# Kernel tuning notes

Hardware: AMD Instinct MI355X
Metric: run time of the kernel (lower is better)

## Reference

```python
import jax, jax.numpy as jnp
import numpy as np

N_NODES = 100000
N_EDGES = 3200000
F_IN = 128
HID = 16
N_CLASSES = 32
N_RELS = 20
BN_EPS = 1e-5


def setup_inputs() -> dict:
    key = jax.random.key(0)
    ks = jax.random.split(key, 14)
    inp = {
        'x': jax.random.normal(ks[0], (N_NODES, F_IN), dtype=jnp.float32),
        'edge_index': jax.random.randint(ks[1], (2, N_EDGES), 0, N_NODES, dtype=jnp.int32),
        'edge_type': jax.random.randint(ks[2], (N_EDGES,), 0, N_RELS, dtype=jnp.int32),
        # conv1 params (relation weights, root weight, bias)
        'W1': jax.random.normal(ks[3], (N_RELS, F_IN, HID), dtype=jnp.float32) / np.sqrt(F_IN),
        'root1': jax.random.normal(ks[4], (F_IN, HID), dtype=jnp.float32) / np.sqrt(F_IN),
        'b1': jnp.zeros((HID,), dtype=jnp.float32),
        # bn1
        'gamma1': jnp.ones((HID,), dtype=jnp.float32),
        'beta1': jnp.zeros((HID,), dtype=jnp.float32),
        # conv2 params
        'W2': jax.random.normal(ks[5], (N_RELS, HID, N_CLASSES), dtype=jnp.float32) / np.sqrt(HID),
        'root2': jax.random.normal(ks[6], (HID, N_CLASSES), dtype=jnp.float32) / np.sqrt(HID),
        'b2': jnp.zeros((N_CLASSES,), dtype=jnp.float32),
        # bn2
        'gamma2': jnp.ones((N_CLASSES,), dtype=jnp.float32),
        'beta2': jnp.zeros((N_CLASSES,), dtype=jnp.float32),
    }
    return inp


def rgcn_conv(x, src, dst, etype, W, Wroot, b):
    # h[r] = x @ W_r  -> [R, N, O]; small O keeps this cheap
    h = jnp.einsum('nf,rfo->rno', x, W)
    msg = h[etype, src]  # [E, O] gather of transformed source features
    # per-(relation, dst-node) in-degree for mean aggregation
    cnt = jnp.zeros((W.shape[0], x.shape[0]), x.dtype).at[etype, dst].add(1.0)
    norm = jnp.where(cnt > 0, 1.0 / jnp.maximum(cnt, 1.0), 0.0)
    msg = msg * norm[etype, dst][:, None]
    out = jnp.zeros((x.shape[0], W.shape[-1]), x.dtype).at[dst].add(msg)
    return out + x @ Wroot + b


def batch_norm(x, gamma, beta):
    # training-mode BatchNorm1d: batch statistics, biased variance
    m = x.mean(axis=0)
    v = x.var(axis=0)
    return (x - m) * jax.lax.rsqrt(v + BN_EPS) * gamma + beta


def reference(x, edge_index, edge_type, W1, root1, b1, gamma1, beta1,
              W2, root2, b2, gamma2, beta2):
    src, dst = edge_index[0], edge_index[1]
    h = rgcn_conv(x, src, dst, edge_type, W1, root1, b1)
    h = jax.nn.relu(batch_norm(h, gamma1, beta1))
    # dropout(0.1) treated as identity (eval mode)
    h = rgcn_conv(h, src, dst, edge_type, W2, root2, b2)
    h = jax.nn.relu(batch_norm(h, gamma2, beta2))
    return jax.nn.log_softmax(h, axis=1)
```

## Files before the change

kernel.cpp:

```cpp
#include <hip/hip_runtime.h>
#include <hip/hip_bf16.h>

#define N_NODES 100000
#define N_EDGES 3200000
#define F_IN 128
#define HID 16
#define N_CLASSES 32
#define N_RELS 20
#define BN_EPS 1e-5f
#define N_CELLS (N_NODES * N_RELS)
#define BIN_SHIFT 13
#define BIN_CELLS 8192
#define NBINS ((N_CELLS + BIN_CELLS - 1) / BIN_CELLS)
#define CHUNK 8192
#define NBLK ((N_EDGES + CHUNK - 1) / CHUNK)
#define HM_N (NBINS * NBLK)
#define HM_NB ((HM_N + 2047) / 2048)
#define SLOT_ELEMS (N_NODES * HID)
#define XPAD 136

#define OFF_CS     0ull
#define OFF_REC    8000000ull
#define OFF_AGG1   20800000ull
#define OFF_HM     27200000ull
#define OFF_BSUM   27584000ull
#define OFF_BINOFF 27588096ull
#define OFF_ST1    27589120ull
#define OFF_ST2    27589376ull
#define OFF_WT     27589632ull
#define OFF_W2T    27675648ull
#define OFF_X      27698176ull
#define SLOT_BYTES 3200000ull

typedef __attribute__((ext_vector_type(8))) short bf16x8;
typedef __attribute__((ext_vector_type(4))) short bf16x4;
typedef __attribute__((ext_vector_type(4))) float f32x4;

__device__ inline short f2bf(float f) {
    union { __hip_bfloat16 h; short s; } u;
    u.h = __float2bfloat16(f);
    return u.s;
}

__device__ inline float bf2f(short s) {
    union { unsigned u; float f; } x;
    x.u = ((unsigned)(unsigned short)s) << 16;
    return x.f;
}


__global__ __launch_bounds__(256) void hist2_kernel(const int* __restrict__ et,
                                                    const int* __restrict__ dst,
                                                    int* __restrict__ hm) {
    __shared__ int lh[NBINS];
    int t = threadIdx.x;
    for (int i = t; i < NBINS; i += 256) lh[i] = 0;
    __syncthreads();
    int e0 = blockIdx.x * CHUNK, e1 = min(e0 + CHUNK, N_EDGES);
    for (int e = e0 + t; e < e1; e += 256) {
        int m = et[e] * N_NODES + dst[e];
        atomicAdd(&lh[m >> BIN_SHIFT], 1);
    }
    __syncthreads();
    for (int i = t; i < NBINS; i += 256) hm[i * NBLK + blockIdx.x] = lh[i];
}

__global__ void scan_k1(const int* __restrict__ a, int* __restrict__ bsum, int n) {
    __shared__ int red[256];
    int base = blockIdx.x * 2048 + threadIdx.x * 8;
    int s = 0;
#pragma unroll
    for (int i = 0; i < 8; ++i) {
        int idx = base + i;
        if (idx < n) s += a[idx];
    }
    red[threadIdx.x] = s;
    __syncthreads();
    for (int off = 128; off > 0; off >>= 1) {
        if (threadIdx.x < off) red[threadIdx.x] += red[threadIdx.x + off];
        __syncthreads();
    }
    if (threadIdx.x == 0) bsum[blockIdx.x] = red[0];
}

__global__ void scan_k2(int* __restrict__ bsum, int nb) {
    __shared__ int p[1024];
    int t = threadIdx.x;
    int v = (t < nb) ? bsum[t] : 0;
    p[t] = v;
    __syncthreads();
    for (int off = 1; off < 1024; off <<= 1) {
        int a = (t >= off) ? p[t - off] : 0;
        __syncthreads();
        p[t] += a;
        __syncthreads();
    }
    if (t < nb) bsum[t] = p[t] - v;
}

__global__ void scan_k3(int* __restrict__ a, const int* __restrict__ bsum, int n) {
    __shared__ int red[256];
    int base = blockIdx.x * 2048 + threadIdx.x * 8;
    int v[8];
    int s = 0;
#pragma unroll
    for (int i = 0; i < 8; ++i) {
        int idx = base + i;
        v[i] = (idx < n) ? a[idx] : 0;
        s += v[i];
    }
    red[threadIdx.x] = s;
    __syncthreads();
    for (int off = 1; off < 256; off <<= 1) {
        int t = (threadIdx.x >= off) ? red[threadIdx.x - off] : 0;
        __syncthreads();
        red[threadIdx.x] += t;
        __syncthreads();
    }
    int run = bsum[blockIdx.x] + red[threadIdx.x] - s;
#pragma unroll
    for (int i = 0; i < 8; ++i) {
        int idx = base + i;
        if (idx < n) a[idx] = run;
        run += v[i];
    }
}

__global__ void binoff_kernel(const int* __restrict__ hm, int* __restrict__ binoff) {
    int t = threadIdx.x;
    if (t < NBINS) binoff[t] = hm[t * NBLK];
    if (t == 0) binoff[NBINS] = N_EDGES;
}

__global__ __launch_bounds__(256) void bucket2_kernel(const int* __restrict__ src,
                                                      const int* __restrict__ dst,
                                                      const int* __restrict__ et,
                                                      const int* __restrict__ hm,
                                                      unsigned long long* __restrict__ bucket) {
    __shared__ int ptr[NBINS];
    int t = threadIdx.x;
    for (int i = t; i < NBINS; i += 256) ptr[i] = hm[i * NBLK + blockIdx.x];
    __syncthreads();
    int e0 = blockIdx.x * CHUNK, e1 = min(e0 + CHUNK, N_EDGES);
    for (int e = e0 + t; e < e1; e += 256) {
        int m = et[e] * N_NODES + dst[e];
        int pos = atomicAdd(&ptr[m >> BIN_SHIFT], 1);
        bucket[pos] = ((unsigned long long)m << 17) | (unsigned)src[e];
    }
}

__global__ __launch_bounds__(256) void place_kernel(const unsigned long long* __restrict__ bucket,
                                                    const int* __restrict__ binoff,
                                                    int* __restrict__ cs,
                                                    unsigned* __restrict__ rec) {
    __shared__ int cnt[BIN_CELLS];
    __shared__ int part[256];
    int b = blockIdx.x;
    int cellbase = b << BIN_SHIFT;
    int ncells = min(BIN_CELLS, N_CELLS - cellbase);
    int ebase = binoff[b], eend = binoff[b + 1];
    int t = threadIdx.x;
    for (int i = t; i < BIN_CELLS; i += 256) cnt[i] = 0;
    __syncthreads();
    for (int e = ebase + t; e < eend; e += 256) {
        int c = (int)(bucket[e] >> 17) - cellbase;
        atomicAdd(&cnt[c], 1);
    }
    __syncthreads();
    int b32 = t * 32;
    int s = 0;
#pragma unroll
    for (int i = 0; i < 32; ++i) s += cnt[b32 + i];
    part[t] = s;
    __syncthreads();
    for (int off = 1; off < 256; off <<= 1) {
        int a = (t >= off) ? part[t - off] : 0;
        __syncthreads();
        part[t] += a;
        __syncthreads();
    }
    int run = (t ? part[t - 1] : 0);
#pragma unroll
    for (int i = 0; i < 32; ++i) { int c = cnt[b32 + i]; cnt[b32 + i] = run; run += c; }
    __syncthreads();
    for (int e = ebase + t; e < eend; e += 256) {
        unsigned long long p = bucket[e];
        int c = (int)(p >> 17) - cellbase;
        int pos = ebase + atomicAdd(&cnt[c], 1);
        rec[pos] = (unsigned)(p & 0x1FFFFull);
    }
    __syncthreads();
    for (int c = t; c < ncells; c += 256) cs[cellbase + c] = ebase + cnt[c];
}


__global__ void wt_convert(const float* __restrict__ W1, const float* __restrict__ root1,
                           __hip_bfloat16* __restrict__ Wt) {
    int r = blockIdx.x;
    const float* src = (r < N_RELS) ? (W1 + (size_t)r * F_IN * HID) : root1;
    for (int i = threadIdx.x; i < F_IN * HID; i += 256) {
        int f = i >> 4, o = i & 15;
        int s = f >> 5, kgrp = (f >> 3) & 3, e = f & 7;
        size_t dst = (((size_t)(r * 4 + s) * 64) + kgrp * 16 + o) * 8 + e;
        Wt[dst] = __float2bfloat16(src[i]);
    }
}

__global__ void wt2_convert(const float* __restrict__ W2, const float* __restrict__ root2,
                            __hip_bfloat16* __restrict__ W2t) {
    int i = blockIdx.x * 256 + threadIdx.x;
    if (i < 11 * 32 * 32) {
        int p = i >> 10, oc = (i >> 5) & 31, k = i & 31;
        float v;
        if (p == 10) v = (k < 16) ? root2[k * N_CLASSES + oc] : 0.f;
        else v = W2[((size_t)(2 * p + (k >> 4)) * HID + (k & 15)) * N_CLASSES + oc];
        W2t[i] = __float2bfloat16(v);
    }
}


__global__ __launch_bounds__(256, 4) void xform_gemm(const float* __restrict__ x,
                                                     const __hip_bfloat16* __restrict__ Wt,
                                                     const float* __restrict__ b1,
                                                     __hip_bfloat16* __restrict__ h1,
                                                     float* __restrict__ agg1) {
    __shared__ __hip_bfloat16 xs[64 * XPAD];
    int t = threadIdx.x;
    int nodeBase = blockIdx.x * 64;

#pragma unroll
    for (int it = 0; it < 4; ++it) {
        int idx = it * 256 + t;
        int ln = idx >> 4;
        int g = (idx & 15) * 8;
        int node = nodeBase + ln;
        float4 a = {0.f, 0.f, 0.f, 0.f}, b = {0.f, 0.f, 0.f, 0.f};
        if (node < N_NODES) {
            const float* xp = x + (size_t)node * F_IN + g;
            a = *(const float4*)xp;
            b = *(const float4*)(xp + 4);
        }
        bf16x8 v;
        v[0] = f2bf(a.x); v[1] = f2bf(a.y); v[2] = f2bf(a.z); v[3] = f2bf(a.w);
        v[4] = f2bf(b.x); v[5] = f2bf(b.y); v[6] = f2bf(b.z); v[7] = f2bf(b.w);
        *(bf16x8*)(&xs[ln * XPAD + g]) = v;
    }
    __syncthreads();

    int lane = t & 63;
    int wave = t >> 6;
    int col = lane & 15;
    int kgrp = lane >> 4;
    int row = wave * 16 + col;
    int node = nodeBase + row;
    bool valid = node < N_NODES;

    bf16x8 xf[4];
#pragma unroll
    for (int s = 0; s < 4; ++s)
        xf[s] = *(const bf16x8*)(&xs[row * XPAD + s * 32 + kgrp * 8]);

    for (int r = 0; r < N_RELS + 1; ++r) {
        f32x4 acc = {0.f, 0.f, 0.f, 0.f};
#pragma unroll
        for (int s = 0; s < 4; ++s) {
            bf16x8 wf = *(const bf16x8*)(Wt + (((size_t)(r * 4 + s) * 64) + lane) * 8);
            acc = __builtin_amdgcn_mfma_f32_16x16x32_bf16(wf, xf[s], acc, 0, 0, 0);
        }
        if (valid) {
            if (r < N_RELS) {
                union { ushort4 u4; short s4[4]; } o;
                o.s4[0] = f2bf(acc[0]); o.s4[1] = f2bf(acc[1]);
                o.s4[2] = f2bf(acc[2]); o.s4[3] = f2bf(acc[3]);
                *(ushort4*)(h1 + ((size_t)r * N_NODES + node) * HID + kgrp * 4) = o.u4;
            } else {
                int c0 = kgrp * 4;
                float4 o = {acc[0] + b1[c0], acc[1] + b1[c0 + 1],
                            acc[2] + b1[c0 + 2], acc[3] + b1[c0 + 3]};
                *(float4*)(agg1 + (size_t)node * HID + c0) = o;
            }
        }
    }
}

__global__ __launch_bounds__(256) void conv1_agg(const __hip_bfloat16* __restrict__ h1,
                                                 const unsigned* __restrict__ rec,
                                                 const int* __restrict__ cs,
                                                 float* __restrict__ agg1,
                                                 float* __restrict__ st1) {
    __shared__ float ls[HID], lq[HID];
    if (threadIdx.x < HID) { ls[threadIdx.x] = 0.f; lq[threadIdx.x] = 0.f; }
    __syncthreads();
    int q = threadIdx.x & 3, slot = threadIdx.x >> 2;
    int d = blockIdx.x * 64 + slot;
    bool valid = d < N_NODES;
    float acc[4] = {0.f, 0.f, 0.f, 0.f};
    if (valid) {
        for (int r = 0; r < N_RELS; ++r) {
            int m = r * N_NODES + d;
            int s0 = (m == 0) ? 0 : cs[m - 1];
            int s1 = cs[m];
            if (s1 > s0) {
                const __hip_bfloat16* hr = h1 + (size_t)r * SLOT_ELEMS + q * 4;
                float pa[4] = {0.f, 0.f, 0.f, 0.f};
                for (int i = s0; i < s1; ++i) {
                    int sn = rec[i];
                    bf16x4 v = *(const bf16x4*)(hr + (size_t)sn * HID);
#pragma unroll
                    for (int k = 0; k < 4; ++k) pa[k] += bf2f(v[k]);
                }
                float inv = 1.0f / (float)(s1 - s0);
#pragma unroll
                for (int k = 0; k < 4; ++k) acc[k] = fmaf(pa[k], inv, acc[k]);
            }
        }
    }
    float vout[4] = {0.f, 0.f, 0.f, 0.f};
    if (valid) {
        float4* ap = (float4*)(agg1 + (size_t)d * HID + q * 4);
        float4 a0 = *ap;
        vout[0] = a0.x + acc[0]; vout[1] = a0.y + acc[1];
        vout[2] = a0.z + acc[2]; vout[3] = a0.w + acc[3];
        *ap = float4{vout[0], vout[1], vout[2], vout[3]};
    }
#pragma unroll
    for (int k = 0; k < 4; ++k) {
        atomicAdd(&ls[q * 4 + k], vout[k]);
        atomicAdd(&lq[q * 4 + k], vout[k] * vout[k]);
    }
    __syncthreads();
    if (threadIdx.x < HID) {
        atomicAdd(&st1[threadIdx.x], ls[threadIdx.x]);
        atomicAdd(&st1[HID + threadIdx.x], lq[threadIdx.x]);
    }
}

__global__ void bn_relu1(const float* __restrict__ a, const float* __restrict__ stats,
                         const float* __restrict__ gamma, const float* __restrict__ beta,
                         __hip_bfloat16* __restrict__ hb) {
    int i = blockIdx.x * 256 + threadIdx.x;
    if (i < N_NODES * HID) {
        int j = i & (HID - 1);
        float mean = stats[j] * (1.0f / N_NODES);
        float var = stats[HID + j] * (1.0f / N_NODES) - mean * mean;
        float rs = rsqrtf(var + BN_EPS);
        float val = (a[i] - mean) * rs * gamma[j] + beta[j];
        hb[i] = __float2bfloat16(fmaxf(val, 0.f));
    }
}


__global__ __launch_bounds__(256) void conv2_agg(const __hip_bfloat16* __restrict__ hbnb,
                                                 const unsigned* __restrict__ rec,
                                                 const int* __restrict__ cs,
                                                 __hip_bfloat16* __restrict__ agg2) {
    int pair = threadIdx.x >> 1, half = threadIdx.x & 1;
    int m = blockIdx.x * 128 + pair;
    if (m >= N_CELLS) return;
    int s0 = (m == 0) ? 0 : cs[m - 1];
    int s1 = cs[m];
    const __hip_bfloat16* hb = hbnb + half * 8;
    float acc[8] = {0.f, 0.f, 0.f, 0.f, 0.f, 0.f, 0.f, 0.f};
    for (int i = s0; i < s1; ++i) {
        int sn = rec[i];
        bf16x8 v = *(const bf16x8*)(hb + (size_t)sn * HID);
#pragma unroll
        for (int k = 0; k < 8; ++k) acc[k] += bf2f(v[k]);
    }
    float inv = (s1 > s0) ? 1.0f / (float)(s1 - s0) : 0.f;
    bf16x8 o;
#pragma unroll
    for (int k = 0; k < 8; ++k) o[k] = f2bf(acc[k] * inv);
    *(bf16x8*)(agg2 + (size_t)m * HID + half * 8) = o;
}

__global__ __launch_bounds__(256) void gemm2(const __hip_bfloat16* __restrict__ agg2,
                                             const __hip_bfloat16* __restrict__ W2t,
                                             const float* __restrict__ b2,
                                             float* __restrict__ buf2) {
    int wave = threadIdx.x >> 6, lane = threadIdx.x & 63;
    int col = lane & 15, kgrp = lane >> 4;
    int node = blockIdx.x * 64 + wave * 16 + col;
    bool valid = node < N_NODES;
    int nidx = valid ? node : 0;

    bf16x8 bf[11];
#pragma unroll
    for (int p = 0; p < 11; ++p) {
        int slot = 2 * p + (kgrp >> 1);
        bf[p] = *(const bf16x8*)(agg2 + ((size_t)slot * N_NODES + nidx) * HID + (kgrp & 1) * 8);
    }
#pragma unroll
    for (int ct = 0; ct < 2; ++ct) {
        f32x4 acc = {0.f, 0.f, 0.f, 0.f};
#pragma unroll
        for (int p = 0; p < 11; ++p) {
            bf16x8 wf = *(const bf16x8*)(W2t + ((size_t)p * 32 + ct * 16 + col) * 32 + kgrp * 8);
            acc = __builtin_amdgcn_mfma_f32_16x16x32_bf16(wf, bf[p], acc, 0, 0, 0);
        }
        if (valid) {
            int c0 = ct * 16 + kgrp * 4;
            float4 o = {acc[0] + b2[c0], acc[1] + b2[c0 + 1],
                        acc[2] + b2[c0 + 2], acc[3] + b2[c0 + 3]};
            *(float4*)(buf2 + (size_t)node * N_CLASSES + c0) = o;
        }
    }
}

template <int CH>
__global__ void bn_stats(const float* __restrict__ v, float* __restrict__ stats) {
    __shared__ float ls[CH], lq[CH];
    if (threadIdx.x < CH) { ls[threadIdx.x] = 0.f; lq[threadIdx.x] = 0.f; }
    __syncthreads();
    const int total = N_NODES * CH;
    int j = threadIdx.x % CH;
    float s = 0.f, q = 0.f;
    for (int i = blockIdx.x * blockDim.x + threadIdx.x; i < total; i += gridDim.x * blockDim.x) {
        float t = v[i];
        s += t; q += t * t;
    }
    atomicAdd(&ls[j], s);
    atomicAdd(&lq[j], q);
    __syncthreads();
    if (threadIdx.x < CH) {
        atomicAdd(&stats[threadIdx.x], ls[threadIdx.x]);
        atomicAdd(&stats[CH + threadIdx.x], lq[threadIdx.x]);
    }
}

__global__ void final_kernel(const float* __restrict__ buf2, const float* __restrict__ stats,
                             const float* __restrict__ gamma, const float* __restrict__ beta,
                             float* __restrict__ out) {
    int idx = blockIdx.x * 256 + threadIdx.x;
    int j = threadIdx.x & 31;
    float mean = stats[j] * (1.0f / N_NODES);
    float var = stats[N_CLASSES + j] * (1.0f / N_NODES) - mean * mean;
    float rs = rsqrtf(var + BN_EPS);
    float v = fmaxf((buf2[idx] - mean) * rs * gamma[j] + beta[j], 0.f);
    float m = v;
#pragma unroll
    for (int o = 16; o >= 1; o >>= 1) m = fmaxf(m, __shfl_xor(m, o, 32));
    float ex = __expf(v - m);
    float ssum = ex;
#pragma unroll
    for (int o = 16; o >= 1; o >>= 1) ssum += __shfl_xor(ssum, o, 32);
    out[idx] = (v - m) - logf(ssum);
}

extern "C" void kernel_launch(void* const* d_in, const int* in_sizes, int n_in,
                              void* d_out, int out_size, void* d_ws, size_t ws_size,
                              hipStream_t stream) {
    const float* x      = (const float*)d_in[0];
    const int*   eidx   = (const int*)d_in[1];
    const int*   etype  = (const int*)d_in[2];
    const float* W1     = (const float*)d_in[3];
    const float* root1  = (const float*)d_in[4];
    const float* b1     = (const float*)d_in[5];
    const float* gamma1 = (const float*)d_in[6];
    const float* beta1  = (const float*)d_in[7];
    const float* W2     = (const float*)d_in[8];
    const float* root2  = (const float*)d_in[9];
    const float* b2     = (const float*)d_in[10];
    const float* gamma2 = (const float*)d_in[11];
    const float* beta2  = (const float*)d_in[12];

    const int* src = eidx;
    const int* dst = eidx + N_EDGES;

    char* ws = (char*)d_ws;
    int*      cs     = (int*)(ws + OFF_CS);
    unsigned* rec    = (unsigned*)(ws + OFF_REC);
    float*    buf2   = (float*)(ws + OFF_REC);
    float*    agg1   = (float*)(ws + OFF_AGG1);
    int*      hm     = (int*)(ws + OFF_HM);
    int*      bsum   = (int*)(ws + OFF_BSUM);
    int*      binoff = (int*)(ws + OFF_BINOFF);
    float*    st1    = (float*)(ws + OFF_ST1);
    float*    st2    = (float*)(ws + OFF_ST2);
    __hip_bfloat16* Wt  = (__hip_bfloat16*)(ws + OFF_WT);
    __hip_bfloat16* W2t = (__hip_bfloat16*)(ws + OFF_W2T);
    unsigned long long* bucket = (unsigned long long*)(ws + OFF_X);
    __hip_bfloat16* rx   = (__hip_bfloat16*)(ws + OFF_X);
    __hip_bfloat16* h1   = rx;
    __hip_bfloat16* hbnb = rx + (size_t)20 * SLOT_ELEMS;
    __hip_bfloat16* agg2 = rx;

    float* out = (float*)d_out;

    hipMemsetAsync(st1, 0, 512, stream);

    hist2_kernel<<<NBLK, 256, 0, stream>>>(etype, dst, hm);
    scan_k1<<<HM_NB, 256, 0, stream>>>(hm, bsum, HM_N);
    scan_k2<<<1, 1024, 0, stream>>>(bsum, HM_NB);
    scan_k3<<<HM_NB, 256, 0, stream>>>(hm, bsum, HM_N);
    binoff_kernel<<<1, 256, 0, stream>>>(hm, binoff);
    bucket2_kernel<<<NBLK, 256, 0, stream>>>(src, dst, etype, hm, bucket);
    place_kernel<<<NBINS, 256, 0, stream>>>(bucket, binoff, cs, rec);

    wt_convert<<<N_RELS + 1, 256, 0, stream>>>(W1, root1, Wt);
    wt2_convert<<<(11 * 32 * 32 + 255) / 256, 256, 0, stream>>>(W2, root2, W2t);

    xform_gemm<<<(N_NODES + 63) / 64, 256, 0, stream>>>(x, Wt, b1, h1, agg1);

    conv1_agg<<<(N_NODES + 63) / 64, 256, 0, stream>>>(h1, rec, cs, agg1, st1);
    bn_relu1<<<(N_NODES * HID + 255) / 256, 256, 0, stream>>>(agg1, st1, gamma1, beta1, hbnb);

    conv2_agg<<<(N_CELLS + 127) / 128, 256, 0, stream>>>(hbnb, rec, cs, agg2);
    gemm2<<<(N_NODES + 63) / 64, 256, 0, stream>>>(agg2, W2t, b2, buf2);
    bn_stats<N_CLASSES><<<512, 256, 0, stream>>>(buf2, st2);
    final_kernel<<<(N_NODES * N_CLASSES + 255) / 256, 256, 0, stream>>>(buf2, st2, gamma2, beta2, out);
}
```

Baseline: 321.4 us.

## Fuse conv2 aggregation, relation GEMM and BN stats; shrink bucket records to 32-bit

Conv2 aggregation, the per-relation weight multiply (now fp32 FMAs with W2 in shared memory instead of MFMA), the root term, bias and BN statistics are merged into one per-node kernel. This removes the 20-slot agg2 intermediate, the separate gemm2 and bn_stats passes, and the W2 conversion kernel. The bucket records for the CSR build are packed into 32 bits using the cell offset within the bin, halving that traffic. In exchange it adds heavy per-thread register use (32 accumulators), about 43KB of shared memory per block, and serial relation loops per node that may limit occupancy and latency hiding.

```diff
diff --git a/kernel.cpp b/kernel.cpp
--- a/kernel.cpp
+++ b/kernel.cpp
@@ -136,7 +136,7 @@
                                                       const int* __restrict__ dst,
                                                       const int* __restrict__ et,
                                                       const int* __restrict__ hm,
-                                                      unsigned long long* __restrict__ bucket) {
+                                                      unsigned* __restrict__ bucket) {
     __shared__ int ptr[NBINS];
     int t = threadIdx.x;
     for (int i = t; i < NBINS; i += 256) ptr[i] = hm[i * NBLK + blockIdx.x];
@@ -145,11 +145,11 @@
     for (int e = e0 + t; e < e1; e += 256) {
         int m = et[e] * N_NODES + dst[e];
         int pos = atomicAdd(&ptr[m >> BIN_SHIFT], 1);
-        bucket[pos] = ((unsigned long long)m << 17) | (unsigned)src[e];
-    }
-}
-
-__global__ __launch_bounds__(256) void place_kernel(const unsigned long long* __restrict__ bucket,
+        bucket[pos] = ((unsigned)(m & (BIN_CELLS - 1)) << 17) | (unsigned)src[e];
+    }
+}
+
+__global__ __launch_bounds__(256) void place_kernel(const unsigned* __restrict__ bucket,
                                                     const int* __restrict__ binoff,
                                                     int* __restrict__ cs,
                                                     unsigned* __restrict__ rec) {
@@ -163,7 +163,7 @@
     for (int i = t; i < BIN_CELLS; i += 256) cnt[i] = 0;
     __syncthreads();
     for (int e = ebase + t; e < eend; e += 256) {
-        int c = (int)(bucket[e] >> 17) - cellbase;
+        int c = (int)(bucket[e] >> 17);
         atomicAdd(&cnt[c], 1);
     }
     __syncthreads();
@@ -184,10 +184,10 @@
     for (int i = 0; i < 32; ++i) { int c = cnt[b32 + i]; cnt[b32 + i] = run; run += c; }
     __syncthreads();
     for (int e = ebase + t; e < eend; e += 256) {
-        unsigned long long p = bucket[e];
-        int c = (int)(p >> 17) - cellbase;
+        unsigned p = bucket[e];
+        int c = (int)(p >> 17);
         int pos = ebase + atomicAdd(&cnt[c], 1);
-        rec[pos] = (unsigned)(p & 0x1FFFFull);
+        rec[pos] = p & 0x1FFFFu;
     }
     __syncthreads();
     for (int c = t; c < ncells; c += 256) cs[cellbase + c] = ebase + cnt[c];
@@ -203,18 +203,6 @@
         int s = f >> 5, kgrp = (f >> 3) & 3, e = f & 7;
         size_t dst = (((size_t)(r * 4 + s) * 64) + kgrp * 16 + o) * 8 + e;
         Wt[dst] = __float2bfloat16(src[i]);
-    }
-}
-
-__global__ void wt2_convert(const float* __restrict__ W2, const float* __restrict__ root2,
-                            __hip_bfloat16* __restrict__ W2t) {
-    int i = blockIdx.x * 256 + threadIdx.x;
-    if (i < 11 * 32 * 32) {
-        int p = i >> 10, oc = (i >> 5) & 31, k = i & 31;
-        float v;
-        if (p == 10) v = (k < 16) ? root2[k * N_CLASSES + oc] : 0.f;
-        else v = W2[((size_t)(2 * p + (k >> 4)) * HID + (k & 15)) * N_CLASSES + oc];
-        W2t[i] = __float2bfloat16(v);
     }
 }
 
@@ -350,81 +338,85 @@
 }
 
 
-__global__ __launch_bounds__(256) void conv2_agg(const __hip_bfloat16* __restrict__ hbnb,
-                                                 const unsigned* __restrict__ rec,
-                                                 const int* __restrict__ cs,
-                                                 __hip_bfloat16* __restrict__ agg2) {
-    int pair = threadIdx.x >> 1, half = threadIdx.x & 1;
-    int m = blockIdx.x * 128 + pair;
-    if (m >= N_CELLS) return;
-    int s0 = (m == 0) ? 0 : cs[m - 1];
-    int s1 = cs[m];
-    const __hip_bfloat16* hb = hbnb + half * 8;
-    float acc[8] = {0.f, 0.f, 0.f, 0.f, 0.f, 0.f, 0.f, 0.f};
-    for (int i = s0; i < s1; ++i) {
-        int sn = rec[i];
-        bf16x8 v = *(const bf16x8*)(hb + (size_t)sn * HID);
-#pragma unroll
-        for (int k = 0; k < 8; ++k) acc[k] += bf2f(v[k]);
-    }
-    float inv = (s1 > s0) ? 1.0f / (float)(s1 - s0) : 0.f;
-    bf16x8 o;
-#pragma unroll
-    for (int k = 0; k < 8; ++k) o[k] = f2bf(acc[k] * inv);
-    *(bf16x8*)(agg2 + (size_t)m * HID + half * 8) = o;
-}
-
-__global__ __launch_bounds__(256) void gemm2(const __hip_bfloat16* __restrict__ agg2,
-                                             const __hip_bfloat16* __restrict__ W2t,
-                                             const float* __restrict__ b2,
-                                             float* __restrict__ buf2) {
-    int wave = threadIdx.x >> 6, lane = threadIdx.x & 63;
-    int col = lane & 15, kgrp = lane >> 4;
-    int node = blockIdx.x * 64 + wave * 16 + col;
-    bool valid = node < N_NODES;
-    int nidx = valid ? node : 0;
-
-    bf16x8 bf[11];
-#pragma unroll
-    for (int p = 0; p < 11; ++p) {
-        int slot = 2 * p + (kgrp >> 1);
-        bf[p] = *(const bf16x8*)(agg2 + ((size_t)slot * N_NODES + nidx) * HID + (kgrp & 1) * 8);
-    }
-#pragma unroll
-    for (int ct = 0; ct < 2; ++ct) {
-        f32x4 acc = {0.f, 0.f, 0.f, 0.f};
-#pragma unroll
-        for (int p = 0; p < 11; ++p) {
-            bf16x8 wf = *(const bf16x8*)(W2t + ((size_t)p * 32 + ct * 16 + col) * 32 + kgrp * 8);
-            acc = __builtin_amdgcn_mfma_f32_16x16x32_bf16(wf, bf[p], acc, 0, 0, 0);
-        }
-        if (valid) {
-            int c0 = ct * 16 + kgrp * 4;
-            float4 o = {acc[0] + b2[c0], acc[1] + b2[c0 + 1],
-                        acc[2] + b2[c0 + 2], acc[3] + b2[c0 + 3]};
-            *(float4*)(buf2 + (size_t)node * N_CLASSES + c0) = o;
-        }
-    }
-}
-
-template <int CH>
-__global__ void bn_stats(const float* __restrict__ v, float* __restrict__ stats) {
-    __shared__ float ls[CH], lq[CH];
-    if (threadIdx.x < CH) { ls[threadIdx.x] = 0.f; lq[threadIdx.x] = 0.f; }
-    __syncthreads();
-    const int total = N_NODES * CH;
-    int j = threadIdx.x % CH;
-    float s = 0.f, q = 0.f;
-    for (int i = blockIdx.x * blockDim.x + threadIdx.x; i < total; i += gridDim.x * blockDim.x) {
-        float t = v[i];
-        s += t; q += t * t;
-    }
-    atomicAdd(&ls[j], s);
-    atomicAdd(&lq[j], q);
-    __syncthreads();
-    if (threadIdx.x < CH) {
-        atomicAdd(&stats[threadIdx.x], ls[threadIdx.x]);
-        atomicAdd(&stats[CH + threadIdx.x], lq[threadIdx.x]);
+__global__ __launch_bounds__(256) void conv2_fused(const __hip_bfloat16* __restrict__ hbnb,
+                                                   const unsigned* __restrict__ rec,
+                                                   const int* __restrict__ cs,
+                                                   const float* __restrict__ W2,
+                                                   const float* __restrict__ root2,
+                                                   const float* __restrict__ b2,
+                                                   float* __restrict__ buf2,
+                                                   float* __restrict__ st2) {
+    __shared__ float w[(N_RELS + 1) * HID * N_CLASSES];
+    __shared__ float ls[N_CLASSES], lq[N_CLASSES];
+    int t = threadIdx.x;
+    for (int i = t; i < N_RELS * HID * N_CLASSES; i += 256) w[i] = W2[i];
+    for (int i = t; i < HID * N_CLASSES; i += 256) w[N_RELS * HID * N_CLASSES + i] = root2[i];
+    if (t < N_CLASSES) { ls[t] = 0.f; lq[t] = 0.f; }
+    __syncthreads();
+
+    int q = t & 3, slot = t >> 2;
+    int d = blockIdx.x * 64 + slot;
+    bool valid = d < N_NODES;
+    float out[N_CLASSES];
+#pragma unroll
+    for (int c = 0; c < N_CLASSES; ++c) out[c] = 0.f;
+
+    if (valid) {
+        for (int r = 0; r < N_RELS; ++r) {
+            int m = r * N_NODES + d;
+            int s0 = (m == 0) ? 0 : cs[m - 1];
+            int s1 = cs[m];
+            if (s1 > s0) {
+                const __hip_bfloat16* hb = hbnb + q * 4;
+                float pa[4] = {0.f, 0.f, 0.f, 0.f};
+                for (int i = s0; i < s1; ++i) {
+                    bf16x4 v = *(const bf16x4*)(hb + (size_t)rec[i] * HID);
+#pragma unroll
+                    for (int k = 0; k < 4; ++k) pa[k] += bf2f(v[k]);
+                }
+                float inv = 1.0f / (float)(s1 - s0);
+                const float* wr = w + (r * HID + q * 4) * N_CLASSES;
+#pragma unroll
+                for (int k = 0; k < 4; ++k) {
+                    float mv = pa[k] * inv;
+#pragma unroll
+                    for (int c = 0; c < N_CLASSES; ++c)
+                        out[c] = fmaf(mv, wr[k * N_CLASSES + c], out[c]);
+                }
+            }
+        }
+        bf16x4 hv = *(const bf16x4*)(hbnb + (size_t)d * HID + q * 4);
+        const float* wr = w + (N_RELS * HID + q * 4) * N_CLASSES;
+#pragma unroll
+        for (int k = 0; k < 4; ++k) {
+            float mv = bf2f(hv[k]);
+#pragma unroll
+            for (int c = 0; c < N_CLASSES; ++c)
+                out[c] = fmaf(mv, wr[k * N_CLASSES + c], out[c]);
+        }
+    }
+#pragma unroll
+    for (int c = 0; c < N_CLASSES; ++c) {
+        out[c] += __shfl_xor(out[c], 1, 64);
+        out[c] += __shfl_xor(out[c], 2, 64);
+    }
+    if (valid) {
+        int c0 = q * 8;
+        float v0[8];
+#pragma unroll
+        for (int k = 0; k < 8; ++k) {
+            v0[k] = out[c0 + k] + b2[c0 + k];
+            atomicAdd(&ls[c0 + k], v0[k]);
+            atomicAdd(&lq[c0 + k], v0[k] * v0[k]);
+        }
+        float4* bp = (float4*)(buf2 + (size_t)d * N_CLASSES + c0);
+        bp[0] = float4{v0[0], v0[1], v0[2], v0[3]};
+        bp[1] = float4{v0[4], v0[5], v0[6], v0[7]};
+    }
+    __syncthreads();
+    if (t < N_CLASSES) {
+        atomicAdd(&st2[t], ls[t]);
+        atomicAdd(&st2[N_CLASSES + t], lq[t]);
     }
 }
 
@@ -470,20 +462,18 @@
     char* ws = (char*)d_ws;
     int*      cs     = (int*)(ws + OFF_CS);
     unsigned* rec    = (unsigned*)(ws + OFF_REC);
-    float*    buf2   = (float*)(ws + OFF_REC);
     float*    agg1   = (float*)(ws + OFF_AGG1);
     int*      hm     = (int*)(ws + OFF_HM);
     int*      bsum   = (int*)(ws + OFF_BSUM);
     int*      binoff = (int*)(ws + OFF_BINOFF);
     float*    st1    = (float*)(ws + OFF_ST1);
     float*    st2    = (float*)(ws + OFF_ST2);
-    __hip_bfloat16* Wt  = (__hip_bfloat16*)(ws + OFF_WT);
-    __hip_bfloat16* W2t = (__hip_bfloat16*)(ws + OFF_W2T);
-    unsigned long long* bucket = (unsigned long long*)(ws + OFF_X);
+    __hip_bfloat16* Wt = (__hip_bfloat16*)(ws + OFF_WT);
+    unsigned* bucket = (unsigned*)(ws + OFF_X);
     __hip_bfloat16* rx   = (__hip_bfloat16*)(ws + OFF_X);
     __hip_bfloat16* h1   = rx;
     __hip_bfloat16* hbnb = rx + (size_t)20 * SLOT_ELEMS;
-    __hip_bfloat16* agg2 = rx;
+    float*    buf2   = (float*)(ws + OFF_X);
 
     float* out = (float*)d_out;
 
@@ -498,15 +488,13 @@
     place_kernel<<<NBINS, 256, 0, stream>>>(bucket, binoff, cs, rec);
 
     wt_convert<<<N_RELS + 1, 256, 0, stream>>>(W1, root1, Wt);
-    wt2_convert<<<(11 * 32 * 32 + 255) / 256, 256, 0, stream>>>(W2, root2, W2t);
 
     xform_gemm<<<(N_NODES + 63) / 64, 256, 0, stream>>>(x, Wt, b1, h1, agg1);
 
     conv1_agg<<<(N_NODES + 63) / 64, 256, 0, stream>>>(h1, rec, cs, agg1, st1);
     bn_relu1<<<(N_NODES * HID + 255) / 256, 256, 0, stream>>>(agg1, st1, gamma1, beta1, hbnb);
 
-    conv2_agg<<<(N_CELLS + 127) / 128, 256, 0, stream>>>(hbnb, rec, cs, agg2);
-    gemm2<<<(N_NODES + 63) / 64, 256, 0, stream>>>(agg2, W2t, b2, buf2);
-    bn_stats<N_CLASSES><<<512, 256, 0, stream>>>(buf2, st2);
+    conv2_fused<<<(N_NODES + 63) / 64, 256, 0, stream>>>(hbnb, rec, cs, W2, root2, b2,
+                                                         buf2, st2);
     final_kernel<<<(N_NODES * N_CLASSES + 255) / 256, 256, 0, stream>>>(buf2, st2, gamma2, beta2, out);
 }
```

Measured after the change: 487.9 us. +51.8%, slower.
